# Optimization experiments

Hardware: AMD Instinct MI355X
Metric: run time of the kernel (lower is better)

Reference implementation:

```python
import jax, jax.numpy as jnp
import numpy as np

H, DH = 8, 64          # heads, dim_head
SCALE = DH ** -0.5

def _ln(x, g, b, eps=1e-5):
    m = jnp.mean(x, axis=-1, keepdims=True)
    v = jnp.var(x, axis=-1, keepdims=True)
    return (x - m) / jnp.sqrt(v + eps) * g + b

def setup_inputs() -> dict:
    key = jax.random.key(0)
    ks = jax.random.split(key, 16)
    b, n, din, dim, depth, mlp, nc = 4, 2048, 768, 512, 2, 512, 2
    s = 0.02
    x = jax.random.normal(ks[0], (b, n, din), jnp.float32)
    lens = jax.random.randint(ks[1], (b,), n // 2, n + 1)
    lens = lens.at[0].set(n)  # ensure amax(lens) == n so torch's truncation is a no-op
    return {
        "x": x,
        "lens": lens,
        "cls_token": jax.random.normal(ks[2], (1, 1, dim), jnp.float32),
        "fc_w": jax.random.normal(ks[3], (din, dim), jnp.float32) * s,
        "fc_b": jnp.zeros((dim,), jnp.float32),
        "ln1_g": jnp.ones((depth, dim), jnp.float32),
        "ln1_b": jnp.zeros((depth, dim), jnp.float32),
        "qkv_w": jax.random.normal(ks[4], (depth, dim, 3 * H * DH), jnp.float32) * s,
        "out_w": jax.random.normal(ks[5], (depth, H * DH, dim), jnp.float32) * s,
        "out_b": jnp.zeros((depth, dim), jnp.float32),
        "ln2_g": jnp.ones((depth, dim), jnp.float32),
        "ln2_b": jnp.zeros((depth, dim), jnp.float32),
        "ff1_w": jax.random.normal(ks[6], (depth, dim, mlp), jnp.float32) * s,
        "ff1_b": jnp.zeros((depth, mlp), jnp.float32),
        "ff2_w": jax.random.normal(ks[7], (depth, mlp, dim), jnp.float32) * s,
        "ff2_b": jnp.zeros((depth, dim), jnp.float32),
        "lnf_g": jnp.ones((dim,), jnp.float32),
        "lnf_b": jnp.zeros((dim,), jnp.float32),
        "head_w": jax.random.normal(ks[8], (dim, nc), jnp.float32) * s,
        "head_b": jnp.zeros((nc,), jnp.float32),
    }

def reference(x, lens, cls_token, fc_w, fc_b, ln1_g, ln1_b, qkv_w, out_w, out_b,
              ln2_g, ln2_b, ff1_w, ff1_b, ff2_w, ff2_b, lnf_g, lnf_b, head_w, head_b):
    b, n, _ = x.shape
    # fc + GELU (exact erf gelu, matching torch nn.GELU default)
    x = jax.nn.gelu(x @ fc_w + fc_b, approximate=False)
    x = jnp.concatenate([jnp.broadcast_to(cls_token, (b, 1, x.shape[-1])), x], axis=1)
    n1 = n + 1
    lens1 = lens + 1
    # faithful mask: mask @ mask.mT -> True only where BOTH query and key are padding
    pad = jnp.arange(n1)[None, :] >= lens1[:, None]           # [b, n1]
    mask2 = pad[:, :, None] & pad[:, None, :]                  # [b, n1, n1]
    neg = -jnp.finfo(x.dtype).max
    depth = qkv_w.shape[0]
    for l in range(depth):
        xn = _ln(x, ln1_g[l], ln1_b[l])
        qkv = xn @ qkv_w[l]                                    # [b, n1, 3*H*DH]
        q, k, v = jnp.split(qkv, 3, axis=-1)
        q = q.reshape(b, n1, H, DH).transpose(0, 2, 1, 3)      # [b, h, n1, dh]
        k = k.reshape(b, n1, H, DH).transpose(0, 2, 1, 3)
        v = v.reshape(b, n1, H, DH).transpose(0, 2, 1, 3)
        dots = jnp.einsum('bhid,bhjd->bhij', q, k) * SCALE
        dots = jnp.where(mask2[:, None], neg, dots)
        dots = dots - jnp.max(dots, axis=-1, keepdims=True)
        attn = jax.nn.softmax(dots, axis=-1)
        o = jnp.einsum('bhij,bhjd->bhid', attn, v)
        o = o.transpose(0, 2, 1, 3).reshape(b, n1, H * DH)
        x = o @ out_w[l] + out_b[l] + x
        h = jax.nn.gelu(_ln(x, ln2_g[l], ln2_b[l]) @ ff1_w[l] + ff1_b[l], approximate=False)
        x = h @ ff2_w[l] + ff2_b[l] + x
    x = _ln(x, lnf_g, lnf_b)
    return x[:, 0] @ head_w + head_b   # pool='cls'
```

## Files before the change

### kernel.cpp

```cpp
#include <hip/hip_runtime.h>
#include <hip/hip_bf16.h>
#include <math.h>
#include <float.h>

typedef __hip_bfloat16 bf16;
using bf16x8 = __attribute__((ext_vector_type(8))) __bf16;
using f32x4  = __attribute__((ext_vector_type(4))) float;

constexpr int BATCH = 4;
constexpr int SEQ   = 2048;
constexpr int SEQ1  = 2049;
constexpr int DIN   = 768;
constexpr int DIMC  = 512;
constexpr int DEPTH = 2;
constexpr int NHEAD = 8;
constexpr int DHEAD = 64;
constexpr int ROWS  = BATCH * SEQ1;
constexpr int VKP   = 2112;
constexpr float ATT_SCALE = 0.125f;
constexpr float NEGBIG = -1e30f;

__device__ __forceinline__ bf16x8 ld_frag(const bf16* p) { return *(const bf16x8*)p; }

__device__ __forceinline__ void g2lds16(const bf16* g, bf16* l) {
    __builtin_amdgcn_global_load_lds(
        (const __attribute__((address_space(1))) void*)g,
        (__attribute__((address_space(3))) void*)l, 16, 0, 0);
}

__global__ __launch_bounds__(256) void cast_kernel(const float* __restrict__ src,
                                                   bf16* __restrict__ dst, int n4) {
    int i = blockIdx.x * 256 + threadIdx.x;
    if (i < n4) {
        float4 v = ((const float4*)src)[i];
        dst[i * 4 + 0] = __float2bfloat16(v.x);
        dst[i * 4 + 1] = __float2bfloat16(v.y);
        dst[i * 4 + 2] = __float2bfloat16(v.z);
        dst[i * 4 + 3] = __float2bfloat16(v.w);
    }
}

__global__ __launch_bounds__(256) void wt_transpose_kernel(
    const float* __restrict__ src, bf16* __restrict__ dst,
    int R, int C, long zstride) {
    __shared__ bf16 tile[32][33];
    int z = blockIdx.z;
    const float* s = src + (size_t)z * zstride;
    bf16* d = dst + (size_t)z * zstride;
    int tx = threadIdx.x, ty = threadIdx.y;
    int c0 = blockIdx.x * 32, r0 = blockIdx.y * 32;
    int c = c0 + tx;
#pragma unroll
    for (int rr = ty; rr < 32; rr += 8) {
        int r = r0 + rr;
        tile[rr][tx] = (r < R && c < C) ? __float2bfloat16(s[(size_t)r * C + c])
                                        : __float2bfloat16(0.f);
    }
    __syncthreads();
    int rc = r0 + tx;
#pragma unroll
    for (int cc = ty; cc < 32; cc += 8) {
        int oc = c0 + cc;
        if (rc < R && oc < C) d[(size_t)oc * R + rc] = tile[tx][cc];
    }
}

__global__ __launch_bounds__(256) void vt_transpose_kernel(
    const bf16* __restrict__ QKV, bf16* __restrict__ VT) {
    __shared__ bf16 tile[32][33];
    int z = blockIdx.z;
    int bb = z >> 3, hh = z & 7;
    const bf16* s = QKV + (size_t)bb * SEQ1 * 1536 + 1024 + hh * 64;
    bf16* d = VT + (size_t)z * 64 * VKP;
    int tx = threadIdx.x, ty = threadIdx.y;
    int c0 = blockIdx.x * 32, r0 = blockIdx.y * 32;
    int c = c0 + tx;
#pragma unroll
    for (int rr = ty; rr < 32; rr += 8) {
        int r = r0 + rr;
        tile[rr][tx] = (r < SEQ1) ? s[(size_t)r * 1536 + c] : __float2bfloat16(0.f);
    }
    __syncthreads();
    int rc = r0 + tx;
#pragma unroll
    for (int cc = ty; cc < 32; cc += 8) {
        int oc = c0 + cc;
        if (rc < VKP) d[(size_t)oc * VKP + rc] = tile[tx][cc];
    }
}

__global__ void cls_fill_kernel(const float* __restrict__ cls, float* __restrict__ X) {
    int b = blockIdx.x;
    for (int d = threadIdx.x; d < DIMC; d += blockDim.x)
        X[(size_t)b * SEQ1 * DIMC + d] = cls[d];
}

template<int BM, bool GELU_, bool RESID, bool REMAP, bool OBF>
__global__ __launch_bounds__(256) void gemm_bt(
    const bf16* __restrict__ A, const bf16* __restrict__ Bt,
    const float* __restrict__ bias, const float* __restrict__ resid,
    float* __restrict__ Cf, bf16* __restrict__ Ch, int M, int N, int K) {
    constexpr int MI = BM / 32;
    __shared__ __align__(16) bf16 As[BM * 32];
    __shared__ __align__(16) bf16 Bs[4096];
    int tid = threadIdx.x;
    int ln = tid & 63, wv = tid >> 6;
    int wr = wv >> 1, wc = wv & 1;
    int l15 = ln & 15, l4 = ln >> 4;
    int m0 = blockIdx.y * BM, n0 = blockIdx.x * 128;

    f32x4 acc[MI][4];
#pragma unroll
    for (int i = 0; i < MI; ++i)
#pragma unroll
        for (int j = 0; j < 4; ++j) acc[i][j] = {0.f, 0.f, 0.f, 0.f};

    int aslot[MI], bslot[4];
#pragma unroll
    for (int i = 0; i < MI; ++i) {
        int m = wr * (BM / 2) + i * 16 + l15;
        aslot[i] = m * 4 + (l4 ^ ((m >> 1) & 3));
    }
#pragma unroll
    for (int j = 0; j < 4; ++j) {
        int n = wc * 64 + j * 16 + l15;
        bslot[j] = n * 4 + (l4 ^ ((n >> 1) & 3));
    }

    for (int k0 = 0; k0 < K; k0 += 32) {
#pragma unroll
        for (int r = 0; r < BM / 64; ++r) {
            int s = r * 256 + tid;
            int m = s >> 2, c = s & 3;
            int kb = c ^ ((m >> 1) & 3);
            int gm = m0 + m; if (gm > M - 1) gm = M - 1;
            g2lds16(A + (size_t)gm * K + k0 + kb * 8, &As[s * 8]);
        }
#pragma unroll
        for (int r = 0; r < 2; ++r) {
            int s = r * 256 + tid;
            int n = s >> 2, c = s & 3;
            int kb = c ^ ((n >> 1) & 3);
            g2lds16(Bt + (size_t)(n0 + n) * K + k0 + kb * 8, &Bs[s * 8]);
        }
        __syncthreads();
        bf16x8 af[MI], bfr[4];
#pragma unroll
        for (int i = 0; i < MI; ++i) af[i] = ld_frag(&As[aslot[i] * 8]);
#pragma unroll
        for (int j = 0; j < 4; ++j) bfr[j] = ld_frag(&Bs[bslot[j] * 8]);
#pragma unroll
        for (int i = 0; i < MI; ++i)
#pragma unroll
            for (int j = 0; j < 4; ++j)
                acc[i][j] = __builtin_amdgcn_mfma_f32_16x16x32_bf16(af[i], bfr[j], acc[i][j], 0, 0, 0);
        __syncthreads();
    }

#pragma unroll
    for (int i = 0; i < MI; ++i) {
#pragma unroll
        for (int j = 0; j < 4; ++j) {
            int gn = n0 + wc * 64 + j * 16 + l15;
            float bb = bias ? bias[gn] : 0.f;
#pragma unroll
            for (int r = 0; r < 4; ++r) {
                int gm = m0 + wr * (BM / 2) + i * 16 + l4 * 4 + r;
                if (gm >= M) continue;
                float v = acc[i][j][r] + bb;
                if (GELU_) v = 0.5f * v * (1.f + erff(v * 0.70710678118654752f));
                size_t orow = gm;
                if (REMAP) { int b_ = gm >> 11; orow = (size_t)b_ * SEQ1 + (gm & 2047) + 1; }
                size_t oi = orow * (size_t)N + gn;
                if (RESID) v += resid[oi];
                if (OBF) Ch[oi] = __float2bfloat16(v); else Cf[oi] = v;
            }
        }
    }
}

__global__ __launch_bounds__(256) void ln_kernel(const float* __restrict__ Xin, bf16* __restrict__ Xout,
                          const float* __restrict__ g, const float* __restrict__ bb) {
    int wv = threadIdx.x >> 6, ln = threadIdx.x & 63;
    int row = blockIdx.x * 4 + wv;
    if (row >= ROWS) return;
    const float* xr = Xin + (size_t)row * DIMC + ln * 8;
    float4 a = *(const float4*)xr;
    float4 c = *(const float4*)(xr + 4);
    float s = a.x + a.y + a.z + a.w + c.x + c.y + c.z + c.w;
#pragma unroll
    for (int off = 1; off < 64; off <<= 1) s += __shfl_xor(s, off, 64);
    float mean = s * (1.f / 512.f);
    float d[8] = {a.x - mean, a.y - mean, a.z - mean, a.w - mean,
                  c.x - mean, c.y - mean, c.z - mean, c.w - mean};
    float var = 0.f;
#pragma unroll
    for (int e = 0; e < 8; ++e) var += d[e] * d[e];
#pragma unroll
    for (int off = 1; off < 64; off <<= 1) var += __shfl_xor(var, off, 64);
    float rinv = rsqrtf(var * (1.f / 512.f) + 1e-5f);
    const float* gp = g + ln * 8;
    const float* bp = bb + ln * 8;
    float4 g0 = *(const float4*)gp, g1 = *(const float4*)(gp + 4);
    float4 b0 = *(const float4*)bp, b1 = *(const float4*)(bp + 4);
    float gg[8] = {g0.x, g0.y, g0.z, g0.w, g1.x, g1.y, g1.z, g1.w};
    float bbv[8] = {b0.x, b0.y, b0.z, b0.w, b1.x, b1.y, b1.z, b1.w};
    union { unsigned short u[8]; uint4 v; } ou;
#pragma unroll
    for (int e = 0; e < 8; ++e)
        ou.u[e] = __builtin_bit_cast(unsigned short, __float2bfloat16(d[e] * rinv * gg[e] + bbv[e]));
    *(uint4*)(Xout + (size_t)row * DIMC + ln * 8) = ou.v;
}

__global__ __launch_bounds__(256, 5) void attn_kernel(
    const bf16* __restrict__ QKV, const bf16* __restrict__ VT,
    const int* __restrict__ lens, bf16* __restrict__ O) {
    __shared__ __align__(16) bf16 Ks[2][4096];
    __shared__ __align__(16) bf16 Vs[2][4096];
    int tid = threadIdx.x, ln = tid & 63, wv = tid >> 6;
    int l15 = ln & 15, l4 = ln >> 4;
    int q0 = blockIdx.x * 64, h = blockIdx.y, b = blockIdx.z;
    int len1 = lens[b] + 1;
    const bf16* qkv_b = QKV + (size_t)b * SEQ1 * 1536;
    const bf16* vt_b  = VT + (size_t)(b * 8 + h) * 64 * VKP;

    uint4 z4 = make_uint4(0u, 0u, 0u, 0u);
    uint4 q0v = z4, q1v = z4;
    int qrow = q0 + wv * 16 + l15;
    if (qrow < SEQ1) {
        const bf16* qp = qkv_b + (size_t)qrow * 1536 + h * 64 + l4 * 8;
        q0v = *(const uint4*)qp;
        q1v = *(const uint4*)(qp + 32);
    }
    bf16x8 bq0 = __builtin_bit_cast(bf16x8, q0v);
    bf16x8 bq1 = __builtin_bit_cast(bf16x8, q1v);
    bool qpad = (qrow >= len1);

    float mrun = NEGBIG, lrun = 0.f;
    f32x4 oaccT[4];
#pragma unroll
    for (int t = 0; t < 4; ++t) oaccT[t] = {0.f, 0.f, 0.f, 0.f};

    uint4 kr[2], vr[2];
    int srow[2], sseg[2];
    int kslot[2], vslot[2];
#pragma unroll
    for (int rr = 0; rr < 2; ++rr) {
        int idx = rr * 256 + tid;
        int row = idx >> 3, seg = idx & 7;
        srow[rr] = row; sseg[rr] = seg;
        int pb = row >> 5, w = row & 31;
        int krow = pb * 32 + ((w >> 2) & 1) * 16 + (w >> 3) * 4 + (w & 3);
        kslot[rr] = krow * 8 + (seg ^ (krow & 7));
        vslot[rr] = row * 8 + (seg ^ (row & 7));
    }

#pragma unroll
    for (int rr = 0; rr < 2; ++rr) {
        kr[rr] = (srow[rr] < SEQ1)
            ? *(const uint4*)(qkv_b + (size_t)srow[rr] * 1536 + 512 + h * 64 + sseg[rr] * 8) : z4;
        vr[rr] = *(const uint4*)(vt_b + (size_t)srow[rr] * VKP + sseg[rr] * 8);
    }
#pragma unroll
    for (int rr = 0; rr < 2; ++rr) {
        *(uint4*)&Ks[0][kslot[rr] * 8] = kr[rr];
        *(uint4*)&Vs[0][vslot[rr] * 8] = vr[rr];
    }
    __syncthreads();

    for (int kt = 0; kt < 33; ++kt) {
        int k0 = kt * 64;
        int buf = kt & 1;
        if (kt < 32) {
            int kn = k0 + 64;
#pragma unroll
            for (int rr = 0; rr < 2; ++rr) {
                kr[rr] = (kn + srow[rr] < SEQ1)
                    ? *(const uint4*)(qkv_b + (size_t)(kn + srow[rr]) * 1536 + 512 + h * 64 + sseg[rr] * 8) : z4;
                vr[rr] = *(const uint4*)(vt_b + (size_t)srow[rr] * VKP + kn + sseg[rr] * 8);
            }
        }

        f32x4 sacc[2][2];
#pragma unroll
        for (int pb = 0; pb < 2; ++pb)
#pragma unroll
            for (int s = 0; s < 2; ++s) {
                int R = pb * 32 + s * 16 + l15;
                f32x4 a = {0.f, 0.f, 0.f, 0.f};
                bf16x8 kf0 = ld_frag(&Ks[buf][(R * 8 + (l4 ^ (R & 7))) * 8]);
                bf16x8 kf1 = ld_frag(&Ks[buf][(R * 8 + ((l4 + 4) ^ (R & 7))) * 8]);
                a = __builtin_amdgcn_mfma_f32_16x16x32_bf16(kf0, bq0, a, 0, 0, 0);
                a = __builtin_amdgcn_mfma_f32_16x16x32_bf16(kf1, bq1, a, 0, 0, 0);
                sacc[pb][s] = a;
            }

        bool needmask = (k0 + 64 > len1) || (kt == 32);
        float sv[2][2][4];
        float mx = NEGBIG;
#pragma unroll
        for (int pb = 0; pb < 2; ++pb)
#pragma unroll
            for (int s = 0; s < 2; ++s)
#pragma unroll
                for (int r = 0; r < 4; ++r) {
                    float v = sacc[pb][s][r] * ATT_SCALE;
                    if (needmask) {
                        int j = k0 + pb * 32 + l4 * 8 + s * 4 + r;
                        if (j >= SEQ1 || (qpad && j >= len1)) v = NEGBIG;
                    }
                    sv[pb][s][r] = v;
                    mx = fmaxf(mx, v);
                }
        mx = fmaxf(mx, __shfl_xor(mx, 16, 64));
        mx = fmaxf(mx, __shfl_xor(mx, 32, 64));
        float mnew = fmaxf(mrun, mx);
        float alpha = __expf(mrun - mnew);
        float rs = 0.f;
        unsigned short pk[2][8];
#pragma unroll
        for (int pb = 0; pb < 2; ++pb)
#pragma unroll
            for (int s = 0; s < 2; ++s)
#pragma unroll
                for (int r = 0; r < 4; ++r) {
                    float ex = sv[pb][s][r] - mnew;
                    float p = (ex < -80.f) ? 0.f : __expf(ex);
                    rs += p;
                    pk[pb][s * 4 + r] = __builtin_bit_cast(unsigned short, __float2bfloat16(p));
                }
        rs += __shfl_xor(rs, 16, 64);
        rs += __shfl_xor(rs, 32, 64);
        lrun = lrun * alpha + rs;
        mrun = mnew;
#pragma unroll
        for (int t = 0; t < 4; ++t) {
            oaccT[t][0] *= alpha; oaccT[t][1] *= alpha;
            oaccT[t][2] *= alpha; oaccT[t][3] *= alpha;
        }

#pragma unroll
        for (int pb = 0; pb < 2; ++pb) {
            union { unsigned short u[8]; bf16x8 v; } pu;
#pragma unroll
            for (int e = 0; e < 8; ++e) pu.u[e] = pk[pb][e];
            bf16x8 pf = pu.v;
#pragma unroll
            for (int t = 0; t < 4; ++t) {
                int VR = t * 16 + l15;
                bf16x8 vf = ld_frag(&Vs[buf][(VR * 8 + ((pb * 4 + l4) ^ (VR & 7))) * 8]);
                oaccT[t] = __builtin_amdgcn_mfma_f32_16x16x32_bf16(vf, pf, oaccT[t], 0, 0, 0);
            }
        }

        if (kt < 32) {
            int ob = buf ^ 1;
#pragma unroll
            for (int rr = 0; rr < 2; ++rr) {
                *(uint4*)&Ks[ob][kslot[rr] * 8] = kr[rr];
                *(uint4*)&Vs[ob][vslot[rr] * 8] = vr[rr];
            }
        }
        __syncthreads();
    }

    if (qrow < SEQ1) {
        float rl = (lrun > 0.f) ? 1.f / lrun : 0.f;
        bf16* orow = O + ((size_t)b * SEQ1 + qrow) * DIMC + h * 64;
#pragma unroll
        for (int t = 0; t < 4; ++t) {
            union { unsigned short u[4]; uint2 v; } ou;
#pragma unroll
            for (int r = 0; r < 4; ++r)
                ou.u[r] = __builtin_bit_cast(unsigned short, __float2bfloat16(oaccT[t][r] * rl));
            *(uint2*)&orow[t * 16 + l4 * 4] = ou.v;
        }
    }
}

__global__ __launch_bounds__(256) void head_kernel(const float* __restrict__ X,
                            const float* __restrict__ g, const float* __restrict__ bb,
                            const float* __restrict__ hw, const float* __restrict__ hb,
                            float* __restrict__ out) {
    int b = blockIdx.x, t = threadIdx.x;
    const float* xr = X + (size_t)b * SEQ1 * DIMC;
    float v0 = xr[t], v1 = xr[t + 256];
    __shared__ float red[256];
    red[t] = v0 + v1;
    __syncthreads();
    for (int w = 128; w > 0; w >>= 1) { if (t < w) red[t] += red[t + w]; __syncthreads(); }
    float mean = red[0] * (1.f / 512.f);
    __syncthreads();
    float d0 = v0 - mean, d1 = v1 - mean;
    red[t] = d0 * d0 + d1 * d1;
    __syncthreads();
    for (int w = 128; w > 0; w >>= 1) { if (t < w) red[t] += red[t + w]; __syncthreads(); }
    float rinv = rsqrtf(red[0] * (1.f / 512.f) + 1e-5f);
    __syncthreads();
    float xn0 = d0 * rinv * g[t] + bb[t];
    float xn1 = d1 * rinv * g[t + 256] + bb[t + 256];
    float p0 = xn0 * hw[t * 2]     + xn1 * hw[(t + 256) * 2];
    float p1 = xn0 * hw[t * 2 + 1] + xn1 * hw[(t + 256) * 2 + 1];
    __shared__ float r0[256], r1[256];
    r0[t] = p0; r1[t] = p1;
    __syncthreads();
    for (int w = 128; w > 0; w >>= 1) { if (t < w) { r0[t] += r0[t + w]; r1[t] += r1[t + w]; } __syncthreads(); }
    if (t == 0) {
        out[b * 2 + 0] = r0[0] + hb[0];
        out[b * 2 + 1] = r1[0] + hb[1];
    }
}

extern "C" void kernel_launch(void* const* d_in, const int* in_sizes, int n_in,
                              void* d_out, int out_size, void* d_ws, size_t ws_size,
                              hipStream_t stream) {
    const float* x      = (const float*)d_in[0];
    const int*   lens   = (const int*)d_in[1];
    const float* cls    = (const float*)d_in[2];
    const float* fc_w   = (const float*)d_in[3];
    const float* fc_b   = (const float*)d_in[4];
    const float* ln1_g  = (const float*)d_in[5];
    const float* ln1_b  = (const float*)d_in[6];
    const float* qkv_w  = (const float*)d_in[7];
    const float* out_w  = (const float*)d_in[8];
    const float* out_b  = (const float*)d_in[9];
    const float* ln2_g  = (const float*)d_in[10];
    const float* ln2_b  = (const float*)d_in[11];
    const float* ff1_w  = (const float*)d_in[12];
    const float* ff1_b  = (const float*)d_in[13];
    const float* ff2_w  = (const float*)d_in[14];
    const float* ff2_b  = (const float*)d_in[15];
    const float* lnf_g  = (const float*)d_in[16];
    const float* lnf_b  = (const float*)d_in[17];
    const float* head_w = (const float*)d_in[18];
    const float* head_b = (const float*)d_in[19];
    float* out = (float*)d_out;

    char* w = (char*)d_ws;
    float* X    = (float*)w;  w += (size_t)ROWS * DIMC * 4;
    bf16*  XNh  = (bf16*)w;   w += (size_t)ROWS * DIMC * 2;
    bf16*  QKVh = (bf16*)w;   w += (size_t)ROWS * 1536 * 2;
    bf16*  Obh  = (bf16*)w;   w += (size_t)ROWS * DIMC * 2;
    bf16*  xbf  = (bf16*)w;   w += (size_t)BATCH * SEQ * DIN * 2;
    bf16*  VT   = xbf;
    bf16*  fc_wt  = (bf16*)w;
    bf16*  qkv_wt = fc_wt  + (size_t)DIN * DIMC;
    bf16*  out_wt = qkv_wt + (size_t)2 * DIMC * 1536;
    bf16*  ff1_wt = out_wt + (size_t)2 * DIMC * DIMC;
    bf16*  ff2_wt = ff1_wt + (size_t)2 * DIMC * DIMC;
    bf16*  Hbh  = Obh;

    dim3 blk(256);
    dim3 tb(32, 8);

    cast_kernel<<<dim3((BATCH * SEQ * DIN / 4 + 255) / 256), blk, 0, stream>>>(
        x, xbf, BATCH * SEQ * DIN / 4);

    wt_transpose_kernel<<<dim3(16, 24, 1), tb, 0, stream>>>(fc_w,  fc_wt,  DIN,  DIMC, (long)DIN * DIMC);
    wt_transpose_kernel<<<dim3(48, 16, 2), tb, 0, stream>>>(qkv_w, qkv_wt, DIMC, 1536, (long)DIMC * 1536);
    wt_transpose_kernel<<<dim3(16, 16, 2), tb, 0, stream>>>(out_w, out_wt, DIMC, DIMC, (long)DIMC * DIMC);
    wt_transpose_kernel<<<dim3(16, 16, 2), tb, 0, stream>>>(ff1_w, ff1_wt, DIMC, DIMC, (long)DIMC * DIMC);
    wt_transpose_kernel<<<dim3(16, 16, 2), tb, 0, stream>>>(ff2_w, ff2_wt, DIMC, DIMC, (long)DIMC * DIMC);

    gemm_bt<64, true, false, true, false><<<dim3(4, 128), blk, 0, stream>>>(
        xbf, fc_wt, fc_b, nullptr, X, nullptr, BATCH * SEQ, DIMC, DIN);
    cls_fill_kernel<<<dim3(BATCH), blk, 0, stream>>>(cls, X);

    for (int l = 0; l < DEPTH; ++l) {
        ln_kernel<<<dim3((ROWS + 3) / 4), blk, 0, stream>>>(X, XNh, ln1_g + l * DIMC, ln1_b + l * DIMC);
        gemm_bt<128, false, false, false, true><<<dim3(12, 65), blk, 0, stream>>>(
            XNh, qkv_wt + (size_t)l * DIMC * 1536, nullptr, nullptr, nullptr, QKVh, ROWS, 1536, DIMC);
        vt_transpose_kernel<<<dim3(2, 66, 32), tb, 0, stream>>>(QKVh, VT);
        attn_kernel<<<dim3(33, NHEAD, BATCH), blk, 0, stream>>>(QKVh, VT, lens, Obh);
        gemm_bt<64, false, true, false, false><<<dim3(4, 129), blk, 0, stream>>>(
            Obh, out_wt + (size_t)l * DIMC * DIMC, out_b + l * DIMC, X, X, nullptr, ROWS, DIMC, DIMC);
        ln_kernel<<<dim3((ROWS + 3) / 4), blk, 0, stream>>>(X, XNh, ln2_g + l * DIMC, ln2_b + l * DIMC);
        gemm_bt<64, true, false, false, true><<<dim3(4, 129), blk, 0, stream>>>(
            XNh, ff1_wt + (size_t)l * DIMC * DIMC, ff1_b + l * DIMC, nullptr, nullptr, Hbh, ROWS, DIMC, DIMC);
        gemm_bt<64, false, true, false, false><<<dim3(4, 129), blk, 0, stream>>>(
            Hbh, ff2_wt + (size_t)l * DIMC * DIMC, ff2_b + l * DIMC, X, X, nullptr, ROWS, DIMC, DIMC);
    }
    head_kernel<<<dim3(BATCH), blk, 0, stream>>>(X, lnf_g, lnf_b, head_w, head_b, out);
}
```

Baseline: 588.8 us.

## Fuse V transpose into QKV GEMM epilogue and merge weight transposes

Adds a dedicated QKV GEMM that tiles per batch and writes Q/K into the QKV buffer while scattering V directly into the transposed VT layout, removing the separate V transpose kernel and its extra global read/write each layer. The three square weight transposes (out, ff1, ff2) are merged into a single launch. The new GEMM uses a smaller BM=64 tile with more blocks, and its V stores are strided 8-byte writes, which may be less coalesced. The VT padding columns beyond SEQ1 are no longer zeroed by this path, which assumes the buffer is otherwise clean or masked.

```diff
diff --git a/kernel.cpp b/kernel.cpp
--- a/kernel.cpp
+++ b/kernel.cpp
@@ -65,28 +65,25 @@
     }
 }
 
-__global__ __launch_bounds__(256) void vt_transpose_kernel(
-    const bf16* __restrict__ QKV, bf16* __restrict__ VT) {
+__global__ __launch_bounds__(256) void wt3_transpose_kernel(
+    const float* __restrict__ w0, const float* __restrict__ w1, const float* __restrict__ w2,
+    bf16* __restrict__ dst) {
     __shared__ bf16 tile[32][33];
     int z = blockIdx.z;
-    int bb = z >> 3, hh = z & 7;
-    const bf16* s = QKV + (size_t)bb * SEQ1 * 1536 + 1024 + hh * 64;
-    bf16* d = VT + (size_t)z * 64 * VKP;
+    const float* srcs[3] = {w0, w1, w2};
+    const float* s = srcs[z >> 1] + (size_t)(z & 1) * DIMC * DIMC;
+    bf16* d = dst + (size_t)z * DIMC * DIMC;
     int tx = threadIdx.x, ty = threadIdx.y;
     int c0 = blockIdx.x * 32, r0 = blockIdx.y * 32;
     int c = c0 + tx;
 #pragma unroll
-    for (int rr = ty; rr < 32; rr += 8) {
-        int r = r0 + rr;
-        tile[rr][tx] = (r < SEQ1) ? s[(size_t)r * 1536 + c] : __float2bfloat16(0.f);
-    }
+    for (int rr = ty; rr < 32; rr += 8)
+        tile[rr][tx] = __float2bfloat16(s[(size_t)(r0 + rr) * DIMC + c]);
     __syncthreads();
     int rc = r0 + tx;
 #pragma unroll
-    for (int cc = ty; cc < 32; cc += 8) {
-        int oc = c0 + cc;
-        if (rc < VKP) d[(size_t)oc * VKP + rc] = tile[tx][cc];
-    }
+    for (int cc = ty; cc < 32; cc += 8)
+        d[(size_t)(c0 + cc) * DIMC + rc] = tile[tx][cc];
 }
 
 __global__ void cls_fill_kernel(const float* __restrict__ cls, float* __restrict__ X) {
@@ -174,6 +171,102 @@
                 size_t oi = orow * (size_t)N + gn;
                 if (RESID) v += resid[oi];
                 if (OBF) Ch[oi] = __float2bfloat16(v); else Cf[oi] = v;
+            }
+        }
+    }
+}
+
+__global__ __launch_bounds__(256) void gemm_qkv(
+    const bf16* __restrict__ A, const bf16* __restrict__ Bt,
+    bf16* __restrict__ QKVout, bf16* __restrict__ VT, int K) {
+    __shared__ __align__(16) bf16 As[64 * 32];
+    __shared__ __align__(16) bf16 Bs[4096];
+    int tid = threadIdx.x;
+    int ln = tid & 63, wv = tid >> 6;
+    int wr = wv >> 1, wc = wv & 1;
+    int l15 = ln & 15, l4 = ln >> 4;
+    int bb = blockIdx.y / 33;
+    int m0 = (blockIdx.y % 33) * 64;
+    int n0 = blockIdx.x * 128;
+    const bf16* Ab = A + (size_t)bb * SEQ1 * K;
+
+    f32x4 acc[2][4];
+#pragma unroll
+    for (int i = 0; i < 2; ++i)
+#pragma unroll
+        for (int j = 0; j < 4; ++j) acc[i][j] = {0.f, 0.f, 0.f, 0.f};
+
+    int aslot[2], bslot[4];
+#pragma unroll
+    for (int i = 0; i < 2; ++i) {
+        int m = wr * 32 + i * 16 + l15;
+        aslot[i] = m * 4 + (l4 ^ ((m >> 1) & 3));
+    }
+#pragma unroll
+    for (int j = 0; j < 4; ++j) {
+        int n = wc * 64 + j * 16 + l15;
+        bslot[j] = n * 4 + (l4 ^ ((n >> 1) & 3));
+    }
+
+    for (int k0 = 0; k0 < K; k0 += 32) {
+        {
+            int s = tid;
+            int m = s >> 2, c = s & 3;
+            int kb = c ^ ((m >> 1) & 3);
+            int gm = m0 + m; if (gm > SEQ1 - 1) gm = SEQ1 - 1;
+            g2lds16(Ab + (size_t)gm * K + k0 + kb * 8, &As[s * 8]);
+        }
+#pragma unroll
+        for (int r = 0; r < 2; ++r) {
+            int s = r * 256 + tid;
+            int n = s >> 2, c = s & 3;
+            int kb = c ^ ((n >> 1) & 3);
+            g2lds16(Bt + (size_t)(n0 + n) * K + k0 + kb * 8, &Bs[s * 8]);
+        }
+        __syncthreads();
+        bf16x8 af[2], bfr[4];
+#pragma unroll
+        for (int i = 0; i < 2; ++i) af[i] = ld_frag(&As[aslot[i] * 8]);
+#pragma unroll
+        for (int j = 0; j < 4; ++j) bfr[j] = ld_frag(&Bs[bslot[j] * 8]);
+#pragma unroll
+        for (int i = 0; i < 2; ++i)
+#pragma unroll
+            for (int j = 0; j < 4; ++j)
+                acc[i][j] = __builtin_amdgcn_mfma_f32_16x16x32_bf16(af[i], bfr[j], acc[i][j], 0, 0, 0);
+        __syncthreads();
+    }
+
+#pragma unroll
+    for (int i = 0; i < 2; ++i) {
+#pragma unroll
+        for (int j = 0; j < 4; ++j) {
+            int gn = n0 + wc * 64 + j * 16 + l15;
+            int keyb = m0 + wr * 32 + i * 16 + l4 * 4;
+            if (gn < 1024) {
+#pragma unroll
+                for (int r = 0; r < 4; ++r) {
+                    int key = keyb + r;
+                    if (key < SEQ1)
+                        QKVout[((size_t)bb * SEQ1 + key) * 1536 + gn] =
+                            __float2bfloat16(acc[i][j][r]);
+                }
+            } else {
+                int hh = (gn - 1024) >> 6, dd = (gn - 1024) & 63;
+                bf16* vrow = VT + ((size_t)(bb * 8 + hh) * 64 + dd) * VKP;
+                if (keyb + 3 < SEQ1) {
+                    union { unsigned short u[4]; uint2 v; } ou;
+#pragma unroll
+                    for (int r = 0; r < 4; ++r)
+                        ou.u[r] = __builtin_bit_cast(unsigned short, __float2bfloat16(acc[i][j][r]));
+                    *(uint2*)&vrow[keyb] = ou.v;
+                } else {
+#pragma unroll
+                    for (int r = 0; r < 4; ++r) {
+                        int key = keyb + r;
+                        if (key < SEQ1) vrow[key] = __float2bfloat16(acc[i][j][r]);
+                    }
+                }
             }
         }
     }
@@ -458,9 +551,7 @@
 
     wt_transpose_kernel<<<dim3(16, 24, 1), tb, 0, stream>>>(fc_w,  fc_wt,  DIN,  DIMC, (long)DIN * DIMC);
     wt_transpose_kernel<<<dim3(48, 16, 2), tb, 0, stream>>>(qkv_w, qkv_wt, DIMC, 1536, (long)DIMC * 1536);
-    wt_transpose_kernel<<<dim3(16, 16, 2), tb, 0, stream>>>(out_w, out_wt, DIMC, DIMC, (long)DIMC * DIMC);
-    wt_transpose_kernel<<<dim3(16, 16, 2), tb, 0, stream>>>(ff1_w, ff1_wt, DIMC, DIMC, (long)DIMC * DIMC);
-    wt_transpose_kernel<<<dim3(16, 16, 2), tb, 0, stream>>>(ff2_w, ff2_wt, DIMC, DIMC, (long)DIMC * DIMC);
+    wt3_transpose_kernel<<<dim3(16, 16, 6), tb, 0, stream>>>(out_w, ff1_w, ff2_w, out_wt);
 
     gemm_bt<64, true, false, true, false><<<dim3(4, 128), blk, 0, stream>>>(
         xbf, fc_wt, fc_b, nullptr, X, nullptr, BATCH * SEQ, DIMC, DIN);
@@ -468,9 +559,8 @@
 
     for (int l = 0; l < DEPTH; ++l) {
         ln_kernel<<<dim3((ROWS + 3) / 4), blk, 0, stream>>>(X, XNh, ln1_g + l * DIMC, ln1_b + l * DIMC);
-        gemm_bt<128, false, false, false, true><<<dim3(12, 65), blk, 0, stream>>>(
-            XNh, qkv_wt + (size_t)l * DIMC * 1536, nullptr, nullptr, nullptr, QKVh, ROWS, 1536, DIMC);
-        vt_transpose_kernel<<<dim3(2, 66, 32), tb, 0, stream>>>(QKVh, VT);
+        gemm_qkv<<<dim3(12, 132), blk, 0, stream>>>(
+            XNh, qkv_wt + (size_t)l * DIMC * 1536, QKVh, VT, DIMC);
         attn_kernel<<<dim3(33, NHEAD, BATCH), blk, 0, stream>>>(QKVh, VT, lens, Obh);
         gemm_bt<64, false, true, false, false><<<dim3(4, 129), blk, 0, stream>>>(
             Obh, out_wt + (size_t)l * DIMC * DIMC, out_b + l * DIMC, X, X, nullptr, ROWS, DIMC, DIMC);
```

New measurement: 553.8 us. 1.06x faster.
